# Performance work log

Measured on AMD Instinct MI355X. Metric: run time of the kernel, lower is better.

## Reference

```python
import jax, jax.numpy as jnp
import numpy as np

PAGE_SIZE = 16
NUM_PAGES = 256
H = 32          # query heads
HKV = 8         # kv heads
D = 128         # head dim
HIDDEN = 4096
SEQ = 2048
ROPE_THETA = 10000.0


def _rope(x, pos):
    # x: [S, h, D], pos: [S]; non-interleaved (rotate-half) RoPE as in
    # flashinfer.rope.apply_rope_pos_ids_inplace / HF Llama.
    half = x.shape[-1] // 2
    inv_freq = 1.0 / (ROPE_THETA ** (jnp.arange(half, dtype=jnp.float32) / half))
    ang = pos.astype(jnp.float32)[:, None] * inv_freq          # [S, half]
    cos = jnp.cos(ang)[:, None, :]
    sin = jnp.sin(ang)[:, None, :]
    x1, x2 = x[..., :half], x[..., half:]
    return jnp.concatenate([x1 * cos - x2 * sin, x2 * cos + x1 * sin], axis=-1).astype(x.dtype)


def setup_inputs() -> dict:
    key = jax.random.key(0)
    ks = jax.random.split(key, 6)
    return {
        "hidden_states": jax.random.normal(ks[0], (1, SEQ, HIDDEN), jnp.float32),
        "position_ids": jnp.arange(SEQ, dtype=jnp.int32),
        "page_indices": jnp.arange(SEQ // PAGE_SIZE, dtype=jnp.int32),  # 128 distinct pages
        "Wq": jax.random.normal(ks[1], (H * D, HIDDEN), jnp.float32) * 0.02,
        "Wk": jax.random.normal(ks[2], (HKV * D, HIDDEN), jnp.float32) * 0.02,
        "Wv": jax.random.normal(ks[3], (HKV * D, HIDDEN), jnp.float32) * 0.02,
        "Wo": jax.random.normal(ks[4], (HIDDEN, H * D), jnp.float32) * 0.02,
        "kv_cache": jnp.zeros((NUM_PAGES, 2, PAGE_SIZE, HKV, D), jnp.float32),
    }


def reference(hidden_states, position_ids, page_indices, Wq, Wk, Wv, Wo, kv_cache):
    S = hidden_states.shape[1]
    x = hidden_states[0]                                  # [S, HIDDEN] (module squeezes batch=1)
    q = (x @ Wq.T).reshape(S, H, D)
    k = (x @ Wk.T).reshape(S, HKV, D)
    v = (x @ Wv.T).reshape(S, HKV, D)
    q = _rope(q, position_ids)
    k = _rope(k, position_ids)

    # Write K/V into the paged cache (page_table.write_block per page)
    n_used = page_indices.shape[0]
    k_pages = k.reshape(n_used, PAGE_SIZE, HKV, D)
    v_pages = v.reshape(n_used, PAGE_SIZE, HKV, D)
    cache = kv_cache.at[page_indices, 0].set(k_pages).at[page_indices, 1].set(v_pages)

    # Gather paged KV back for attention (BatchPrefillWithPagedKVCache)
    kk = cache[page_indices, 0].reshape(-1, HKV, D)[:S]   # [S, HKV, D]
    vv = cache[page_indices, 1].reshape(-1, HKV, D)[:S]

    # GQA: expand kv heads to query heads
    group = H // HKV
    k_rep = jnp.repeat(kk, group, axis=1)                 # [S, H, D]
    v_rep = jnp.repeat(vv, group, axis=1)

    scale = D ** -0.5
    scores = jnp.einsum('qhd,khd->hqk', q * scale, k_rep)  # [H, S, S]
    causal = jnp.arange(S)[:, None] >= jnp.arange(S)[None, :]
    scores = jnp.where(causal[None], scores, jnp.finfo(scores.dtype).min)
    probs = jax.nn.softmax(scores, axis=-1)
    attn = jnp.einsum('hqk,khd->qhd', probs, v_rep)        # [S, H, D]

    out = attn.reshape(S, H * D) @ Wo.T                    # o_proj
    return out[None]                                       # [1, S, HIDDEN]
```

## Files before the change

### kernel.cpp

```cpp
#include <hip/hip_runtime.h>
#include <hip/hip_bf16.h>
#include <math.h>

#define SEQ    2048
#define HIDDEN 4096
#define NH     32
#define NKV    8
#define HD     128
#define QKV_N  6144

typedef __attribute__((ext_vector_type(8))) short bf16x8;
typedef __attribute__((ext_vector_type(4))) float f32x4;
typedef unsigned short u16;

__device__ inline void gl_lds16(const void* g, void* lds) {
  __builtin_amdgcn_global_load_lds((const __attribute__((address_space(1))) void*)g,
                                   (__attribute__((address_space(3))) void*)lds, 16, 0, 0);
}

__device__ inline u16 f2bf(float f) {
  __hip_bfloat16 h = __float2bfloat16(f);
  return *(u16*)&h;
}
__device__ inline float bf2f(u16 u) {
  __hip_bfloat16 h = *(__hip_bfloat16*)&u;
  return __bfloat162float(h);
}

__global__ void cvt_f32_bf16(const float* __restrict__ src, u16* __restrict__ dst, int n8) {
  int i = blockIdx.x * blockDim.x + threadIdx.x;
  if (i >= n8) return;
  const float4* s = (const float4*)src + (size_t)i * 2;
  float4 a = s[0], b = s[1];
  float v[8] = {a.x, a.y, a.z, a.w, b.x, b.y, b.z, b.w};
  union { u16 o[8]; uint4 u; } pk;
#pragma unroll
  for (int j = 0; j < 8; j++) pk.o[j] = f2bf(v[j]);
  *(uint4*)(dst + (size_t)i * 8) = pk.u;
}

template <int OUTF32>
__global__ __launch_bounds__(256) void gemm_bt(const u16* __restrict__ A,
                                               const u16* __restrict__ B,
                                               void* __restrict__ Cout,
                                               int M, int N, int K) {
  __shared__ __align__(16) u16 As[128 * 32];
  __shared__ __align__(16) u16 Bs[128 * 32];
  const int tid = threadIdx.x;
  const int wave = tid >> 6, lane = tid & 63;
  const int quad = lane >> 4, l16 = lane & 15;
  const int wm = wave >> 1, wn = wave & 1;
  const int m0 = blockIdx.y * 128, n0 = blockIdx.x * 128;

  f32x4 acc[4][4] = {};
  const int lrow = lane >> 2;
  const int kchunk = (lane & 3) * 8;

  for (int k0 = 0; k0 < K; k0 += 32) {
    __syncthreads();
#pragma unroll
    for (int i = 0; i < 2; i++) {
      int r = wave * 32 + i * 16 + lrow;
      gl_lds16(A + (size_t)(m0 + r) * K + k0 + kchunk, &As[(wave * 32 + i * 16) * 32]);
      gl_lds16(B + (size_t)(n0 + r) * K + k0 + kchunk, &Bs[(wave * 32 + i * 16) * 32]);
    }
    __syncthreads();
    bf16x8 af[4], bfr[4];
#pragma unroll
    for (int t = 0; t < 4; t++) {
      af[t]  = *(const bf16x8*)&As[(wm * 64 + t * 16 + l16) * 32 + quad * 8];
      bfr[t] = *(const bf16x8*)&Bs[(wn * 64 + t * 16 + l16) * 32 + quad * 8];
    }
#pragma unroll
    for (int mt = 0; mt < 4; mt++)
#pragma unroll
      for (int nt = 0; nt < 4; nt++)
        acc[mt][nt] = __builtin_amdgcn_mfma_f32_16x16x32_bf16(af[mt], bfr[nt], acc[mt][nt], 0, 0, 0);
  }

#pragma unroll
  for (int mt = 0; mt < 4; mt++)
#pragma unroll
    for (int nt = 0; nt < 4; nt++)
#pragma unroll
      for (int r = 0; r < 4; r++) {
        int row = m0 + wm * 64 + mt * 16 + quad * 4 + r;
        int col = n0 + wn * 64 + nt * 16 + l16;
        float v = acc[mt][nt][r];
        if (OUTF32) ((float*)Cout)[(size_t)row * N + col] = v;
        else        ((u16*)Cout)[(size_t)row * N + col] = f2bf(v);
      }
}

__global__ void rope_kernel(u16* __restrict__ qkv, const int* __restrict__ pos_ids) {
  int idx = blockIdx.x * blockDim.x + threadIdx.x;
  int d = idx & 63;
  int h = (idx >> 6) % 40;
  int s = idx / (64 * 40);
  if (s >= SEQ) return;
  int off = (h < NH) ? h * HD : HIDDEN + (h - NH) * HD;
  u16* base = qkv + (size_t)s * QKV_N + off;
  float inv_freq = powf(10000.0f, -(float)d * (1.0f / 64.0f));
  float ang = (float)pos_ids[s] * inv_freq;
  float sn, cs;
  sincosf(ang, &sn, &cs);
  float x1 = bf2f(base[d]);
  float x2 = bf2f(base[d + 64]);
  base[d]      = f2bf(x1 * cs - x2 * sn);
  base[d + 64] = f2bf(x2 * cs + x1 * sn);
}

__global__ __launch_bounds__(256) void transpose_v(const u16* __restrict__ qkv,
                                                   u16* __restrict__ vt) {
  __shared__ u16 t[64][72];
  const int s0 = blockIdx.x * 64, c0 = blockIdx.y * 64;
  const int tid = threadIdx.x;
#pragma unroll
  for (int i = 0; i < 2; i++) {
    int r = (tid >> 3) + i * 32;
    int c = (tid & 7) * 8;
    *(uint4*)&t[r][c] = *(const uint4*)&qkv[(size_t)(s0 + r) * QKV_N + 5120 + c0 + c];
  }
  __syncthreads();
#pragma unroll
  for (int i = 0; i < 2; i++) {
    int c = (tid >> 3) + i * 32;
    int s = (tid & 7) * 8;
    union { uint4 u; u16 e[8]; } o;
#pragma unroll
    for (int j = 0; j < 8; j++) o.e[j] = t[s + j][c];
    *(uint4*)&vt[(size_t)(c0 + c) * SEQ + s0 + s] = o.u;
  }
}

#define PS_STRIDE 72
#define EX_STRIDE 132
__global__ __launch_bounds__(128, 3) void attn_kernel(const u16* __restrict__ qkv,
                                                      const u16* __restrict__ vt,
                                                      u16* __restrict__ attn_out) {
  __shared__ __align__(16) u16 Ps[2][32 * PS_STRIDE];
  __shared__ __align__(16) float Ex[32 * EX_STRIDE];
  const int blk = blockIdx.x;
  const int it = 63 - (blk >> 5);
  const int h  = blk & 31;
  const int kvh = h >> 2;
  const int tid = threadIdx.x;
  const int wave = tid >> 6, lane = tid & 63;
  const int quad = lane >> 4, l16 = lane & 15;
  const int q0 = it * 32;

  const float c = 0.08838834764831845f * 1.4426950408889634f;

  bf16x8 qf[2][4];
#pragma unroll
  for (int m = 0; m < 2; m++)
#pragma unroll
    for (int dc = 0; dc < 4; dc++)
      qf[m][dc] = *(const bf16x8*)(qkv + (size_t)(q0 + m * 16 + l16) * QKV_N + h * HD + dc * 32 + quad * 8);

  const u16* kp[4];
#pragma unroll
  for (int st = 0; st < 4; st++)
    kp[st] = qkv + (size_t)(wave * 64 + st * 16 + l16) * QKV_N + HIDDEN + kvh * HD + quad * 8;
  const u16* vp[8];
#pragma unroll
  for (int dt = 0; dt < 8; dt++)
    vp[dt] = vt + (size_t)(kvh * HD + dt * 16 + l16) * SEQ + wave * 64 + quad * 8;

  float lsum[2][4] = {};
  f32x4 o[2][8] = {};

  const int n_kt = (q0 + 95) >> 6;
  for (int kt = wave; kt < n_kt; kt += 2) {
    const bool last = (kt == n_kt - 1);

    f32x4 s[2][4] = {};
#pragma unroll
    for (int st = 0; st < 4; st++) {
      bf16x8 kst[4];
#pragma unroll
      for (int dc = 0; dc < 4; dc++) kst[dc] = *(const bf16x8*)(kp[st] + dc * 32);
#pragma unroll
      for (int dc = 0; dc < 4; dc++)
#pragma unroll
        for (int m = 0; m < 2; m++)
          s[m][st] = __builtin_amdgcn_mfma_f32_16x16x32_bf16(qf[m][dc], kst[dc], s[m][st], 0, 0, 0);
    }

#pragma unroll
    for (int m = 0; m < 2; m++)
#pragma unroll
      for (int r = 0; r < 4; r++) {
#pragma unroll
        for (int st = 0; st < 4; st++) {
          float v = fmaf(s[m][st][r], c, -32.0f);
          if (last) {
            int key = kt * 64 + st * 16 + l16;
            int row = q0 + m * 16 + quad * 4 + r;
            if (key > row) v = -1e30f;
          }
          float p = exp2f(v);
          s[m][st][r] = p;
          lsum[m][r] += p;
          Ps[wave][(m * 16 + quad * 4 + r) * PS_STRIDE + st * 16 + l16] = f2bf(p);
        }
      }

    bf16x8 pf[2][2];
#pragma unroll
    for (int m = 0; m < 2; m++)
#pragma unroll
      for (int kc = 0; kc < 2; kc++)
        pf[m][kc] = *(const bf16x8*)&Ps[wave][(m * 16 + l16) * PS_STRIDE + kc * 32 + quad * 8];

#pragma unroll
    for (int dt = 0; dt < 8; dt++) {
      bf16x8 vf0 = *(const bf16x8*)(vp[dt]);
      bf16x8 vf1 = *(const bf16x8*)(vp[dt] + 32);
#pragma unroll
      for (int m = 0; m < 2; m++) {
        o[m][dt] = __builtin_amdgcn_mfma_f32_16x16x32_bf16(pf[m][0], vf0, o[m][dt], 0, 0, 0);
        o[m][dt] = __builtin_amdgcn_mfma_f32_16x16x32_bf16(pf[m][1], vf1, o[m][dt], 0, 0, 0);
      }
    }

#pragma unroll
    for (int st = 0; st < 4; st++) kp[st] += (size_t)128 * QKV_N;
#pragma unroll
    for (int dt = 0; dt < 8; dt++) vp[dt] += 128;
  }

#pragma unroll
  for (int m = 0; m < 2; m++)
#pragma unroll
    for (int r = 0; r < 4; r++)
#pragma unroll
      for (int off = 1; off < 16; off <<= 1)
        lsum[m][r] += __shfl_xor(lsum[m][r], off);

  if (wave == 1) {
#pragma unroll
    for (int m = 0; m < 2; m++)
#pragma unroll
      for (int dt = 0; dt < 8; dt++)
#pragma unroll
        for (int r = 0; r < 4; r++)
          Ex[(m * 16 + quad * 4 + r) * EX_STRIDE + dt * 16 + l16] = o[m][dt][r];
    if (l16 == 0) {
#pragma unroll
      for (int m = 0; m < 2; m++)
#pragma unroll
        for (int r = 0; r < 4; r++)
          Ex[(m * 16 + quad * 4 + r) * EX_STRIDE + 128] = lsum[m][r];
    }
  }
  __syncthreads();
  if (wave == 0) {
#pragma unroll
    for (int m = 0; m < 2; m++) {
      float inv[4];
#pragma unroll
      for (int r = 0; r < 4; r++) {
        float lt = lsum[m][r] + Ex[(m * 16 + quad * 4 + r) * EX_STRIDE + 128];
        inv[r] = 1.0f / lt;
      }
#pragma unroll
      for (int dt = 0; dt < 8; dt++)
#pragma unroll
        for (int r = 0; r < 4; r++) {
          int row = q0 + m * 16 + quad * 4 + r;
          float ov = o[m][dt][r] + Ex[(m * 16 + quad * 4 + r) * EX_STRIDE + dt * 16 + l16];
          attn_out[(size_t)row * HIDDEN + h * HD + dt * 16 + l16] = f2bf(ov * inv[r]);
        }
    }
  }
}

extern "C" void kernel_launch(void* const* d_in, const int* in_sizes, int n_in,
                              void* d_out, int out_size, void* d_ws, size_t ws_size,
                              hipStream_t stream) {
  const float* x  = (const float*)d_in[0];
  const int* pos  = (const int*)d_in[1];
  const float* Wq = (const float*)d_in[3];
  const float* Wk = (const float*)d_in[4];
  const float* Wv = (const float*)d_in[5];
  const float* Wo = (const float*)d_in[6];
  float* out = (float*)d_out;

  u16* x_bf    = (u16*)d_ws;
  u16* Wqkv_bf = x_bf + (size_t)SEQ * HIDDEN;
  u16* qkv_bf  = Wqkv_bf + (size_t)QKV_N * HIDDEN;
  u16* attn_bf = qkv_bf + (size_t)SEQ * QKV_N;
  u16* Wo_bf   = attn_bf + (size_t)SEQ * HIDDEN;
  u16* vt_bf   = x_bf;

  auto cvt = [&](const float* s, u16* d, size_t n) {
    int n8 = (int)(n / 8);
    cvt_f32_bf16<<<(n8 + 255) / 256, 256, 0, stream>>>(s, d, n8);
  };
  cvt(x,  x_bf,    (size_t)SEQ * HIDDEN);
  cvt(Wq, Wqkv_bf,                         (size_t)4096 * 4096);
  cvt(Wk, Wqkv_bf + (size_t)4096 * 4096,   (size_t)1024 * 4096);
  cvt(Wv, Wqkv_bf + (size_t)5120 * 4096,   (size_t)1024 * 4096);
  cvt(Wo, Wo_bf,   (size_t)4096 * 4096);

  dim3 g1(QKV_N / 128, SEQ / 128);
  gemm_bt<0><<<g1, 256, 0, stream>>>(x_bf, Wqkv_bf, qkv_bf, SEQ, QKV_N, HIDDEN);

  int rope_threads = SEQ * 40 * 64;
  rope_kernel<<<rope_threads / 256, 256, 0, stream>>>(qkv_bf, pos);

  dim3 gt(SEQ / 64, 1024 / 64);
  transpose_v<<<gt, 256, 0, stream>>>(qkv_bf, vt_bf);

  attn_kernel<<<2048, 128, 0, stream>>>(qkv_bf, vt_bf, attn_bf);

  dim3 g3(HIDDEN / 128, SEQ / 128);
  gemm_bt<1><<<g3, 256, 0, stream>>>(attn_bf, Wo_bf, out, SEQ, HIDDEN, HIDDEN);
}
```

Measured before the change: 639.9 us.

## Transpose attention MFMAs to keep P in registers via shuffles

Swaps the operand order of both attention MFMAs so score and output tiles come out transposed, with each lane holding four consecutive keys for one query row. The softmax probabilities are packed to bf16 pairs in registers and redistributed with cross-lane shuffles instead of a round trip through LDS. Row sums then reduce with two shuffles instead of four, and the final output is written as 8-byte vector stores. Block-to-head mapping is also changed so blocks sharing a KV head are adjacent, aiming for better cache reuse of K/V. The shuffle selection logic adds ALU work and must exactly match the MFMA fragment layout to stay correct.

```diff
diff --git a/kernel.cpp b/kernel.cpp
--- a/kernel.cpp
+++ b/kernel.cpp
@@ -12,6 +12,7 @@
 typedef __attribute__((ext_vector_type(8))) short bf16x8;
 typedef __attribute__((ext_vector_type(4))) float f32x4;
 typedef unsigned short u16;
+typedef unsigned int u32;
 
 __device__ inline void gl_lds16(const void* g, void* lds) {
   __builtin_amdgcn_global_load_lds((const __attribute__((address_space(1))) void*)g,
@@ -133,17 +134,15 @@
   }
 }
 
-#define PS_STRIDE 72
-#define EX_STRIDE 132
 __global__ __launch_bounds__(128, 3) void attn_kernel(const u16* __restrict__ qkv,
                                                       const u16* __restrict__ vt,
                                                       u16* __restrict__ attn_out) {
-  __shared__ __align__(16) u16 Ps[2][32 * PS_STRIDE];
-  __shared__ __align__(16) float Ex[32 * EX_STRIDE];
+  __shared__ __align__(16) float Ex[32 * 132];
   const int blk = blockIdx.x;
+  const int kvh = blk & 7;
+  const int hg = (blk >> 3) & 3;
   const int it = 63 - (blk >> 5);
-  const int h  = blk & 31;
-  const int kvh = h >> 2;
+  const int h  = kvh * 4 + hg;
   const int tid = threadIdx.x;
   const int wave = tid >> 6, lane = tid & 63;
   const int quad = lane >> 4, l16 = lane & 15;
@@ -167,51 +166,67 @@
   for (int dt = 0; dt < 8; dt++)
     vp[dt] = vt + (size_t)(kvh * HD + dt * 16 + l16) * SEQ + wave * 64 + quad * 8;
 
-  float lsum[2][4] = {};
+  float lsum[2] = {0.f, 0.f};
   f32x4 o[2][8] = {};
+
+  const int srcA = ((lane >> 4) & 1) * 32 + l16;
+  const int srcB = srcA + 16;
+  const bool hi = quad >= 2;
 
   const int n_kt = (q0 + 95) >> 6;
   for (int kt = wave; kt < n_kt; kt += 2) {
     const bool last = (kt == n_kt - 1);
 
-    f32x4 s[2][4] = {};
+    u32 pk[2][4][2];
 #pragma unroll
     for (int st = 0; st < 4; st++) {
       bf16x8 kst[4];
 #pragma unroll
       for (int dc = 0; dc < 4; dc++) kst[dc] = *(const bf16x8*)(kp[st] + dc * 32);
+      f32x4 s[2] = {};
 #pragma unroll
       for (int dc = 0; dc < 4; dc++)
 #pragma unroll
         for (int m = 0; m < 2; m++)
-          s[m][st] = __builtin_amdgcn_mfma_f32_16x16x32_bf16(qf[m][dc], kst[dc], s[m][st], 0, 0, 0);
-    }
-
+          s[m] = __builtin_amdgcn_mfma_f32_16x16x32_bf16(kst[dc], qf[m][dc], s[m], 0, 0, 0);
+#pragma unroll
+      for (int m = 0; m < 2; m++) {
+        float pr[4];
+#pragma unroll
+        for (int r = 0; r < 4; r++) {
+          float v = fmaf(s[m][r], c, -32.0f);
+          if (last) {
+            int key = kt * 64 + st * 16 + quad * 4 + r;
+            if (key > q0 + m * 16 + l16) v = -1e30f;
+          }
+          pr[r] = exp2f(v);
+          lsum[m] += pr[r];
+        }
+        pk[m][st][0] = ((u32)f2bf(pr[1]) << 16) | f2bf(pr[0]);
+        pk[m][st][1] = ((u32)f2bf(pr[3]) << 16) | f2bf(pr[2]);
+      }
+    }
+
+    bf16x8 pf[2][2];
 #pragma unroll
     for (int m = 0; m < 2; m++)
 #pragma unroll
-      for (int r = 0; r < 4; r++) {
-#pragma unroll
-        for (int st = 0; st < 4; st++) {
-          float v = fmaf(s[m][st][r], c, -32.0f);
-          if (last) {
-            int key = kt * 64 + st * 16 + l16;
-            int row = q0 + m * 16 + quad * 4 + r;
-            if (key > row) v = -1e30f;
-          }
-          float p = exp2f(v);
-          s[m][st][r] = p;
-          lsum[m][r] += p;
-          Ps[wave][(m * 16 + quad * 4 + r) * PS_STRIDE + st * 16 + l16] = f2bf(p);
-        }
-      }
-
-    bf16x8 pf[2][2];
-#pragma unroll
-    for (int m = 0; m < 2; m++)
-#pragma unroll
-      for (int kc = 0; kc < 2; kc++)
-        pf[m][kc] = *(const bf16x8*)&Ps[wave][(m * 16 + l16) * PS_STRIDE + kc * 32 + quad * 8];
+      for (int kc = 0; kc < 2; kc++) {
+        union { u32 w[4]; bf16x8 v; } u;
+        u32 a0 = (u32)__shfl((int)pk[m][2 * kc][0],     srcA);
+        u32 b0 = (u32)__shfl((int)pk[m][2 * kc + 1][0], srcA);
+        u32 a1 = (u32)__shfl((int)pk[m][2 * kc][1],     srcA);
+        u32 b1 = (u32)__shfl((int)pk[m][2 * kc + 1][1], srcA);
+        u32 a2 = (u32)__shfl((int)pk[m][2 * kc][0],     srcB);
+        u32 b2 = (u32)__shfl((int)pk[m][2 * kc + 1][0], srcB);
+        u32 a3 = (u32)__shfl((int)pk[m][2 * kc][1],     srcB);
+        u32 b3 = (u32)__shfl((int)pk[m][2 * kc + 1][1], srcB);
+        u.w[0] = hi ? b0 : a0;
+        u.w[1] = hi ? b1 : a1;
+        u.w[2] = hi ? b2 : a2;
+        u.w[3] = hi ? b3 : a3;
+        pf[m][kc] = u.v;
+      }
 
 #pragma unroll
     for (int dt = 0; dt < 8; dt++) {
@@ -219,8 +234,8 @@
       bf16x8 vf1 = *(const bf16x8*)(vp[dt] + 32);
 #pragma unroll
       for (int m = 0; m < 2; m++) {
-        o[m][dt] = __builtin_amdgcn_mfma_f32_16x16x32_bf16(pf[m][0], vf0, o[m][dt], 0, 0, 0);
-        o[m][dt] = __builtin_amdgcn_mfma_f32_16x16x32_bf16(pf[m][1], vf1, o[m][dt], 0, 0, 0);
+        o[m][dt] = __builtin_amdgcn_mfma_f32_16x16x32_bf16(vf0, pf[m][0], o[m][dt], 0, 0, 0);
+        o[m][dt] = __builtin_amdgcn_mfma_f32_16x16x32_bf16(vf1, pf[m][1], o[m][dt], 0, 0, 0);
       }
     }
 
@@ -231,47 +246,39 @@
   }
 
 #pragma unroll
-  for (int m = 0; m < 2; m++)
-#pragma unroll
-    for (int r = 0; r < 4; r++)
-#pragma unroll
-      for (int off = 1; off < 16; off <<= 1)
-        lsum[m][r] += __shfl_xor(lsum[m][r], off);
+  for (int m = 0; m < 2; m++) {
+    lsum[m] += __shfl_xor(lsum[m], 16);
+    lsum[m] += __shfl_xor(lsum[m], 32);
+  }
 
   if (wave == 1) {
 #pragma unroll
-    for (int m = 0; m < 2; m++)
+    for (int m = 0; m < 2; m++) {
 #pragma unroll
       for (int dt = 0; dt < 8; dt++)
-#pragma unroll
-        for (int r = 0; r < 4; r++)
-          Ex[(m * 16 + quad * 4 + r) * EX_STRIDE + dt * 16 + l16] = o[m][dt][r];
-    if (l16 == 0) {
-#pragma unroll
-      for (int m = 0; m < 2; m++)
-#pragma unroll
-        for (int r = 0; r < 4; r++)
-          Ex[(m * 16 + quad * 4 + r) * EX_STRIDE + 128] = lsum[m][r];
+        *(f32x4*)&Ex[(m * 16 + l16) * 132 + dt * 16 + quad * 4] = o[m][dt];
+      if (lane < 16) Ex[(m * 16 + l16) * 132 + 128] = lsum[m];
     }
   }
   __syncthreads();
   if (wave == 0) {
 #pragma unroll
     for (int m = 0; m < 2; m++) {
-      float inv[4];
-#pragma unroll
-      for (int r = 0; r < 4; r++) {
-        float lt = lsum[m][r] + Ex[(m * 16 + quad * 4 + r) * EX_STRIDE + 128];
-        inv[r] = 1.0f / lt;
-      }
-#pragma unroll
-      for (int dt = 0; dt < 8; dt++)
-#pragma unroll
-        for (int r = 0; r < 4; r++) {
-          int row = q0 + m * 16 + quad * 4 + r;
-          float ov = o[m][dt][r] + Ex[(m * 16 + quad * 4 + r) * EX_STRIDE + dt * 16 + l16];
-          attn_out[(size_t)row * HIDDEN + h * HD + dt * 16 + l16] = f2bf(ov * inv[r]);
-        }
+      float lt = lsum[m] + Ex[(m * 16 + l16) * 132 + 128];
+      float inv = 1.0f / lt;
+      size_t base = (size_t)(q0 + m * 16 + l16) * HIDDEN + h * HD;
+#pragma unroll
+      for (int dt = 0; dt < 8; dt++) {
+        f32x4 p = *(const f32x4*)&Ex[(m * 16 + l16) * 132 + dt * 16 + quad * 4];
+        float v0 = (o[m][dt][0] + p[0]) * inv;
+        float v1 = (o[m][dt][1] + p[1]) * inv;
+        float v2 = (o[m][dt][2] + p[2]) * inv;
+        float v3 = (o[m][dt][3] + p[3]) * inv;
+        u32 w0 = ((u32)f2bf(v1) << 16) | f2bf(v0);
+        u32 w1 = ((u32)f2bf(v3) << 16) | f2bf(v2);
+        uint2 wv; wv.x = w0; wv.y = w1;
+        *(uint2*)&attn_out[base + dt * 16 + quad * 4] = wv;
+      }
     }
   }
 }
```

Measured after the change: 639.5 us. About the same (-0.1%).
